# Optimization experiments

Measured on AMD Instinct MI355X. Metric: run time of the kernel, lower is better.

The kernel has to match this reference:

```python
import jax, jax.numpy as jnp
import numpy as np

S, B, I, H, O = 1024, 64, 512, 2048, 512


def setup_inputs() -> dict:
    key = jax.random.key(0)
    k1, k2, k3, k4, k5 = jax.random.split(key, 5)
    X = jax.random.normal(k1, (S, B, I), dtype=jnp.float32)
    W_ih = jax.random.normal(k2, (H, I), dtype=jnp.float32) * (1.0 / np.sqrt(I))
    hh = jax.random.uniform(k3, (H,), dtype=jnp.float32)  # clamped-to-[-1,1] diagonal recurrence
    W_ho = jax.random.normal(k4, (O, H), dtype=jnp.float32) * (1.0 / np.sqrt(H))
    b_ho = jax.random.normal(k5, (O,), dtype=jnp.float32) * 0.01
    return {"X": X, "W_ih": W_ih, "hh": hh, "W_ho": W_ho, "b_ho": b_ho}


def reference(X, W_ih, hh, W_ho, b_ho):
    # Batch the input->hidden projection over the whole sequence in one GEMM:
    # u[s,b,h] = X[s,b,i] @ W_ih[h,i]^T
    u = jnp.einsum('sbi,hi->sbh', X, W_ih)
    h0 = jnp.zeros((X.shape[1], W_ih.shape[0]), dtype=X.dtype)

    def step(h, u_t):
        h_new = jnp.abs(u_t + hh * h)
        return h_new, None

    h_final, _ = jax.lax.scan(step, h0, u)
    Y = h_final @ W_ho.T + b_ho  # [B, O]
    return Y
```

## Files before the change

kernel.cpp:

```cpp
#include <hip/hip_runtime.h>
#include <hip/hip_bf16.h>
#include <stdint.h>

#define S_LEN 1024
#define B_SZ  64
#define I_SZ  512
#define H_SZ  2048
#define O_SZ  512
#define BH    (B_SZ * H_SZ)

typedef __bf16  bf16x8 __attribute__((ext_vector_type(8)));
typedef float   f32x4  __attribute__((ext_vector_type(4)));

static __device__ __forceinline__ ushort f2bf(float f) {
  union { float f; unsigned u; } v; v.f = f;
  unsigned r = v.u + 0x7FFFu + ((v.u >> 16) & 1u);
  return (ushort)(r >> 16);
}
static __device__ __forceinline__ float bf2f(ushort u) {
  return __builtin_bit_cast(float, (unsigned)u << 16);
}

#define GLOAD_LDS16(gp, lp) \
  __builtin_amdgcn_global_load_lds( \
      (__attribute__((address_space(1))) void*)(gp), \
      (__attribute__((address_space(3))) void*)(lp), 16, 0, 0)

__global__ __launch_bounds__(256) void convert_transpose_x_kernel(
    const float* __restrict__ X, ushort* __restrict__ XT) {
  int r = blockIdx.x * 2 + (threadIdx.x >> 7);
  int t = threadIdx.x & 127;
  int s = r >> 6, b = r & 63;
  float4 v = *(const float4*)&X[(size_t)r * I_SZ + t * 4];
  ushort4 o;
  o.x = f2bf(v.x); o.y = f2bf(v.y); o.z = f2bf(v.z); o.w = f2bf(v.w);
  *(ushort4*)&XT[((size_t)b * S_LEN + s) * I_SZ + t * 4] = o;
}

__global__ __launch_bounds__(256) void convert_f32_bf16_kernel(
    const float4* __restrict__ in, ushort4* __restrict__ out, int n4) {
  int i = blockIdx.x * 256 + threadIdx.x;
  if (i >= n4) return;
  float4 v = in[i];
  ushort4 o; o.x = f2bf(v.x); o.y = f2bf(v.y); o.z = f2bf(v.z); o.w = f2bf(v.w);
  out[i] = o;
}

__global__ __launch_bounds__(256, 4) void fused_gemm_scan_kernel(
    const ushort* __restrict__ XT,
    const ushort* __restrict__ Wbf,
    const float* __restrict__ hh,
    float* __restrict__ hstate) {
  __shared__ __align__(16) ushort smem[16896];
  ushort* As = smem;
  ushort* Bs = smem + 8192;
  ushort* Cs = smem;

  const int tid  = threadIdx.x;
  const int wave = tid >> 6;
  const int lane = tid & 63;

  const int bid = blockIdx.x;
  const int x = bid & 7;
  const int g = bid >> 3;
  const int b  = (x << 3) | (g & 7);
  const int ht = g >> 3;

  const int wm = (wave >> 1) * 64;
  const int wn = (wave & 1) * 64;
  const int ml = lane & 15;
  const int q  = lane >> 4;

  const int r0     = wave * 32;
  const int srow   = lane >> 3;
  const int schunk = ((lane & 7) - srow) & 7;
  const ushort* gA0 = XT + ((size_t)b * S_LEN + r0 + srow) * I_SZ + schunk * 8;
  const ushort* gB  = Wbf + (size_t)(ht * 128 + r0 + srow) * I_SZ + schunk * 8;
  ushort* lA = As + r0 * 64;
  ushort* lB = Bs + r0 * 64;

  int swz[2];
  swz[0] = ((q + ml) & 7) * 8;
  swz[1] = ((4 + q + ml) & 7) * 8;
  int arow[4], brow[4];
  #pragma unroll
  for (int i = 0; i < 4; ++i) {
    arow[i] = (wm + i * 16 + ml) * 64;
    brow[i] = (wn + i * 16 + ml) * 64;
  }

  float c = 0.0f, p = 0.0f;
  if (tid < 128) c = hh[ht * 128 + tid];

  for (int st = 0; st < 8; ++st) {
    f32x4 acc[4][4] = {};
    const ushort* gA = gA0 + (size_t)st * 128 * I_SZ;

    for (int kt = 0; kt < I_SZ / 64; ++kt) {
      __syncthreads();
      #pragma unroll
      for (int jj = 0; jj < 4; ++jj) {
        GLOAD_LDS16(gA + (size_t)(jj * 8) * I_SZ + kt * 64, lA + jj * 512);
        GLOAD_LDS16(gB + (size_t)(jj * 8) * I_SZ + kt * 64, lB + jj * 512);
      }
      __syncthreads();
      #pragma unroll
      for (int ks = 0; ks < 2; ++ks) {
        bf16x8 af[4], bfr[4];
        #pragma unroll
        for (int i = 0; i < 4; ++i) {
          af[i]  = *(const bf16x8*)&As[arow[i] + swz[ks]];
          bfr[i] = *(const bf16x8*)&Bs[brow[i] + swz[ks]];
        }
        #pragma unroll
        for (int mi = 0; mi < 4; ++mi)
          #pragma unroll
          for (int ni = 0; ni < 4; ++ni)
            acc[mi][ni] = __builtin_amdgcn_mfma_f32_16x16x32_bf16(
                af[mi], bfr[ni], acc[mi][ni], 0, 0, 0);
      }
    }

    __syncthreads();
    const int sb = wm + q * 4;
    #pragma unroll
    for (int mi = 0; mi < 4; ++mi) {
      #pragma unroll
      for (int ni = 0; ni < 4; ++ni) {
        ushort4 o;
        o.x = f2bf(acc[mi][ni][0]); o.y = f2bf(acc[mi][ni][1]);
        o.z = f2bf(acc[mi][ni][2]); o.w = f2bf(acc[mi][ni][3]);
        *(ushort4*)&Cs[(wn + ni * 16 + ml) * 132 + sb + mi * 16] = o;
      }
    }
    __syncthreads();

    if (tid < 128) {
      const ushort* col = &Cs[tid * 132];
      #pragma unroll
      for (int s0 = 0; s0 < 128; s0 += 16) {
        ushort4 v0 = *(const ushort4*)&col[s0];
        ushort4 v1 = *(const ushort4*)&col[s0 + 4];
        ushort4 v2 = *(const ushort4*)&col[s0 + 8];
        ushort4 v3 = *(const ushort4*)&col[s0 + 12];
        p = fmaf(c, fabsf(p), bf2f(v0.x)); p = fmaf(c, fabsf(p), bf2f(v0.y));
        p = fmaf(c, fabsf(p), bf2f(v0.z)); p = fmaf(c, fabsf(p), bf2f(v0.w));
        p = fmaf(c, fabsf(p), bf2f(v1.x)); p = fmaf(c, fabsf(p), bf2f(v1.y));
        p = fmaf(c, fabsf(p), bf2f(v1.z)); p = fmaf(c, fabsf(p), bf2f(v1.w));
        p = fmaf(c, fabsf(p), bf2f(v2.x)); p = fmaf(c, fabsf(p), bf2f(v2.y));
        p = fmaf(c, fabsf(p), bf2f(v2.z)); p = fmaf(c, fabsf(p), bf2f(v2.w));
        p = fmaf(c, fabsf(p), bf2f(v3.x)); p = fmaf(c, fabsf(p), bf2f(v3.y));
        p = fmaf(c, fabsf(p), bf2f(v3.z)); p = fmaf(c, fabsf(p), bf2f(v3.w));
      }
    }
  }

  if (tid < 128) hstate[(size_t)b * H_SZ + ht * 128 + tid] = fabsf(p);
}

__global__ __launch_bounds__(256) void init_y_kernel(
    const float* __restrict__ bho, float* __restrict__ Y) {
  int idx = blockIdx.x * 256 + threadIdx.x;
  Y[idx] = bho[idx & (O_SZ - 1)];
}

__global__ __launch_bounds__(256) void final_tiled_kernel(
    const float* __restrict__ hstate, const float* __restrict__ Who,
    float* __restrict__ Y) {
  __shared__ float Ws[64 * 68];
  __shared__ float Hs[64 * 68];
  const int tid = threadIdx.x;
  const int og = blockIdx.x, kc = blockIdx.y;
  const int to = tid & 15, tb = tid >> 4;
  float acc[4][4] = {};
  #pragma unroll
  for (int ks = 0; ks < 2; ++ks) {
    const int k0 = kc * 128 + ks * 64;
    const int r = tid >> 2, cg = (tid & 3) * 16;
    #pragma unroll
    for (int i2 = 0; i2 < 4; ++i2) {
      *(float4*)&Ws[r * 68 + cg + i2 * 4] =
          *(const float4*)&Who[(size_t)(og * 64 + r) * H_SZ + k0 + cg + i2 * 4];
      *(float4*)&Hs[r * 68 + cg + i2 * 4] =
          *(const float4*)&hstate[(size_t)r * H_SZ + k0 + cg + i2 * 4];
    }
    __syncthreads();
    #pragma unroll 4
    for (int k = 0; k < 64; ++k) {
      float wv[4], hv[4];
      #pragma unroll
      for (int jj2 = 0; jj2 < 4; ++jj2) wv[jj2] = Ws[(to * 4 + jj2) * 68 + k];
      #pragma unroll
      for (int ii = 0; ii < 4; ++ii) hv[ii] = Hs[(tb * 4 + ii) * 68 + k];
      #pragma unroll
      for (int ii = 0; ii < 4; ++ii)
        #pragma unroll
        for (int jj2 = 0; jj2 < 4; ++jj2)
          acc[ii][jj2] += hv[ii] * wv[jj2];
    }
    __syncthreads();
  }
  #pragma unroll
  for (int ii = 0; ii < 4; ++ii)
    #pragma unroll
    for (int jj2 = 0; jj2 < 4; ++jj2)
      atomicAdd(&Y[(size_t)(tb * 4 + ii) * O_SZ + og * 64 + to * 4 + jj2],
                acc[ii][jj2]);
}

extern "C" void kernel_launch(void* const* d_in, const int* in_sizes, int n_in,
                              void* d_out, int out_size, void* d_ws, size_t ws_size,
                              hipStream_t stream) {
  (void)in_sizes; (void)n_in; (void)out_size; (void)ws_size;
  const float* X   = (const float*)d_in[0];
  const float* Wih = (const float*)d_in[1];
  const float* hh  = (const float*)d_in[2];
  const float* Who = (const float*)d_in[3];
  const float* bho = (const float*)d_in[4];
  float* Y = (float*)d_out;

  const size_t XBF = (size_t)S_LEN * B_SZ * I_SZ * 2;
  const size_t WBF = (size_t)H_SZ * I_SZ * 2;

  char* w = (char*)d_ws;
  ushort* XT     = (ushort*)w;
  ushort* Wbf    = (ushort*)(w + XBF);
  float*  hstate = (float*) (w + XBF + WBF);

  convert_transpose_x_kernel<<<(S_LEN * B_SZ) / 2, 256, 0, stream>>>(X, XT);
  {
    int n4w = (int)((size_t)H_SZ * I_SZ / 4);
    convert_f32_bf16_kernel<<<n4w / 256, 256, 0, stream>>>(
        (const float4*)Wih, (ushort4*)Wbf, n4w);
  }

  fused_gemm_scan_kernel<<<1024, 256, 0, stream>>>(XT, Wbf, hh, hstate);

  init_y_kernel<<<(B_SZ * O_SZ) / 256, 256, 0, stream>>>(bho, Y);
  final_tiled_kernel<<<dim3(O_SZ / 64, 16), 256, 0, stream>>>(hstate, Who, Y);
}
```

Baseline: 441.3 us.

## Fuse X fp32-to-bf16 conversion and transpose into the GEMM-scan kernel

```diff
diff --git a/kernel.cpp b/kernel.cpp
--- a/kernel.cpp
+++ b/kernel.cpp
@@ -25,17 +25,6 @@
   __builtin_amdgcn_global_load_lds( \
       (__attribute__((address_space(1))) void*)(gp), \
       (__attribute__((address_space(3))) void*)(lp), 16, 0, 0)
-
-__global__ __launch_bounds__(256) void convert_transpose_x_kernel(
-    const float* __restrict__ X, ushort* __restrict__ XT) {
-  int r = blockIdx.x * 2 + (threadIdx.x >> 7);
-  int t = threadIdx.x & 127;
-  int s = r >> 6, b = r & 63;
-  float4 v = *(const float4*)&X[(size_t)r * I_SZ + t * 4];
-  ushort4 o;
-  o.x = f2bf(v.x); o.y = f2bf(v.y); o.z = f2bf(v.z); o.w = f2bf(v.w);
-  *(ushort4*)&XT[((size_t)b * S_LEN + s) * I_SZ + t * 4] = o;
-}
 
 __global__ __launch_bounds__(256) void convert_f32_bf16_kernel(
     const float4* __restrict__ in, ushort4* __restrict__ out, int n4) {
@@ -46,14 +35,14 @@
   out[i] = o;
 }
 
-__global__ __launch_bounds__(256, 4) void fused_gemm_scan_kernel(
-    const ushort* __restrict__ XT,
+__global__ __launch_bounds__(256, 3) void fused_gemm_scan_kernel(
+    const float* __restrict__ X,
     const ushort* __restrict__ Wbf,
     const float* __restrict__ hh,
     float* __restrict__ hstate) {
-  __shared__ __align__(16) ushort smem[16896];
+  __shared__ __align__(16) ushort smem[17408];
   ushort* As = smem;
-  ushort* Bs = smem + 8192;
+  ushort* Bs = smem + 9216;
   ushort* Cs = smem;
 
   const int tid  = threadIdx.x;
@@ -71,37 +60,68 @@
   const int ml = lane & 15;
   const int q  = lane >> 4;
 
+  const int arow0 = wave * 32 + (lane >> 3);
+  const size_t offA = (size_t)arow0 * (B_SZ * I_SZ) + (size_t)b * I_SZ + (lane & 7) * 8;
+
   const int r0     = wave * 32;
   const int srow   = lane >> 3;
   const int schunk = ((lane & 7) - srow) & 7;
-  const ushort* gA0 = XT + ((size_t)b * S_LEN + r0 + srow) * I_SZ + schunk * 8;
-  const ushort* gB  = Wbf + (size_t)(ht * 128 + r0 + srow) * I_SZ + schunk * 8;
-  ushort* lA = As + r0 * 64;
+  const ushort* gB = Wbf + (size_t)(ht * 128 + r0 + srow) * I_SZ + schunk * 8;
   ushort* lB = Bs + r0 * 64;
 
-  int swz[2];
-  swz[0] = ((q + ml) & 7) * 8;
-  swz[1] = ((4 + q + ml) & 7) * 8;
+  int aoff[2], boff[2];
+  aoff[0] = q * 8;
+  aoff[1] = (4 + q) * 8;
+  boff[0] = ((q + ml) & 7) * 8;
+  boff[1] = ((4 + q + ml) & 7) * 8;
   int arow[4], brow[4];
   #pragma unroll
   for (int i = 0; i < 4; ++i) {
-    arow[i] = (wm + i * 16 + ml) * 64;
+    arow[i] = (wm + i * 16 + ml) * 72;
     brow[i] = (wn + i * 16 + ml) * 64;
   }
 
   float c = 0.0f, p = 0.0f;
   if (tid < 128) c = hh[ht * 128 + tid];
 
+  float4 ar[8];
+  {
+    const float* gp = X + offA;
+    #pragma unroll
+    for (int j = 0; j < 4; ++j) {
+      ar[2 * j]     = *(const float4*)(gp + (size_t)j * (8 * B_SZ * I_SZ));
+      ar[2 * j + 1] = *(const float4*)(gp + (size_t)j * (8 * B_SZ * I_SZ) + 4);
+    }
+  }
+
   for (int st = 0; st < 8; ++st) {
     f32x4 acc[4][4] = {};
-    const ushort* gA = gA0 + (size_t)st * 128 * I_SZ;
 
     for (int kt = 0; kt < I_SZ / 64; ++kt) {
       __syncthreads();
       #pragma unroll
-      for (int jj = 0; jj < 4; ++jj) {
-        GLOAD_LDS16(gA + (size_t)(jj * 8) * I_SZ + kt * 64, lA + jj * 512);
+      for (int j = 0; j < 4; ++j) {
+        union { __bf16 h[8]; uint4 v; } uvt;
+        uvt.h[0] = (__bf16)ar[2 * j].x;     uvt.h[1] = (__bf16)ar[2 * j].y;
+        uvt.h[2] = (__bf16)ar[2 * j].z;     uvt.h[3] = (__bf16)ar[2 * j].w;
+        uvt.h[4] = (__bf16)ar[2 * j + 1].x; uvt.h[5] = (__bf16)ar[2 * j + 1].y;
+        uvt.h[6] = (__bf16)ar[2 * j + 1].z; uvt.h[7] = (__bf16)ar[2 * j + 1].w;
+        *(uint4*)&As[(arow0 + j * 8) * 72 + (lane & 7) * 8] = uvt.v;
+      }
+      #pragma unroll
+      for (int jj = 0; jj < 4; ++jj)
         GLOAD_LDS16(gB + (size_t)(jj * 8) * I_SZ + kt * 64, lB + jj * 512);
+      {
+        int nst = (kt == 7) ? st + 1 : st;
+        int nkt = (kt == 7) ? 0 : kt + 1;
+        if (nst < 8) {
+          const float* gp = X + offA + (size_t)nst * (128 * B_SZ * I_SZ) + nkt * 64;
+          #pragma unroll
+          for (int j = 0; j < 4; ++j) {
+            ar[2 * j]     = *(const float4*)(gp + (size_t)j * (8 * B_SZ * I_SZ));
+            ar[2 * j + 1] = *(const float4*)(gp + (size_t)j * (8 * B_SZ * I_SZ) + 4);
+          }
+        }
       }
       __syncthreads();
       #pragma unroll
@@ -109,9 +129,12 @@
         bf16x8 af[4], bfr[4];
         #pragma unroll
         for (int i = 0; i < 4; ++i) {
-          af[i]  = *(const bf16x8*)&As[arow[i] + swz[ks]];
-          bfr[i] = *(const bf16x8*)&Bs[brow[i] + swz[ks]];
+          af[i]  = *(const bf16x8*)&As[arow[i] + (ks * 4) * 8 + aoff[0] - q * 8 + q * 8];
+          bfr[i] = *(const bf16x8*)&Bs[brow[i] + boff[ks]];
         }
+        #pragma unroll
+        for (int i = 0; i < 4; ++i)
+          af[i] = *(const bf16x8*)&As[arow[i] + (ks * 4 + q) * 8];
         #pragma unroll
         for (int mi = 0; mi < 4; ++mi)
           #pragma unroll
@@ -219,22 +242,19 @@
   const float* bho = (const float*)d_in[4];
   float* Y = (float*)d_out;
 
-  const size_t XBF = (size_t)S_LEN * B_SZ * I_SZ * 2;
   const size_t WBF = (size_t)H_SZ * I_SZ * 2;
 
   char* w = (char*)d_ws;
-  ushort* XT     = (ushort*)w;
-  ushort* Wbf    = (ushort*)(w + XBF);
-  float*  hstate = (float*) (w + XBF + WBF);
-
-  convert_transpose_x_kernel<<<(S_LEN * B_SZ) / 2, 256, 0, stream>>>(X, XT);
+  ushort* Wbf    = (ushort*)w;
+  float*  hstate = (float*) (w + WBF);
+
   {
     int n4w = (int)((size_t)H_SZ * I_SZ / 4);
     convert_f32_bf16_kernel<<<n4w / 256, 256, 0, stream>>>(
         (const float4*)Wih, (ushort4*)Wbf, n4w);
   }
 
-  fused_gemm_scan_kernel<<<1024, 256, 0, stream>>>(XT, Wbf, hh, hstate);
+  fused_gemm_scan_kernel<<<1024, 256, 0, stream>>>(X, Wbf, hh, hstate);
 
   init_y_kernel<<<(B_SZ * O_SZ) / 256, 256, 0, stream>>>(bho, Y);
   final_tiled_kernel<<<dim3(O_SZ / 64, 16), 256, 0, stream>>>(hstate, Who, Y);
```

Measured after the change: 385.8 us. 1.14x faster.
